# Kernel tuning notes

Hardware: AMD Instinct MI355X
Metric: run time of the kernel (lower is better)

The kernel has to match this reference:

```python
import jax, jax.numpy as jnp
import numpy as np
import math

HIDDEN = 768
KEY = 128      # attention_key_size
INTER = 1536   # intermediate_size
B, S = 4, 2048


def setup_inputs() -> dict:
    key = jax.random.key(0)
    ks = jax.random.split(key, 8)
    hidden_states = jax.random.normal(ks[0], (B, S, HIDDEN), dtype=jnp.float32)
    attention_mask = jax.random.randint(ks[1], (B, 1, 1, S), 0, 2, dtype=jnp.int32)
    position_ids = jnp.arange(B * S, dtype=jnp.int32).reshape(B, S) % S
    Wi = jax.random.normal(ks[2], (HIDDEN, 2 * INTER + KEY), dtype=jnp.float32) * 0.02
    bi = jnp.zeros((2 * INTER + KEY,), dtype=jnp.float32)
    gamma = jax.random.normal(ks[3], (2, KEY), dtype=jnp.float32) * 0.02 + 1.0
    beta = jnp.zeros((2, KEY), dtype=jnp.float32)
    Wo = jax.random.normal(ks[4], (INTER, HIDDEN), dtype=jnp.float32) * 0.02
    bo = jnp.zeros((HIDDEN,), dtype=jnp.float32)
    return {"hidden_states": hidden_states, "attention_mask": attention_mask,
            "position_ids": position_ids, "Wi": Wi, "bi": bi,
            "gamma": gamma, "beta": beta, "Wo": Wo, "bo": bo}


def _gau_forward(hidden_states, attention_mask, Wi, bi, gamma, beta, Wo, bo):
    # i_dense + swish activation
    h = jax.nn.silu(jnp.einsum('bsd,de->bse', hidden_states, Wi) + bi)
    u = h[..., :INTER]
    v = h[..., INTER:2 * INTER]
    qk = h[..., 2 * INTER:]
    # OffsetScale: per-head affine (heads=2 -> q, k)
    q = qk * gamma[0] + beta[0]
    k = qk * gamma[1] + beta[1]
    scores = jnp.einsum('bid,bjd->bij', q, k) / math.sqrt(KEY)
    # additive mask: (1 - m) * -1e12, squeeze head dim
    am = (1.0 - attention_mask.astype(scores.dtype)) * -1e12
    scores = scores + am[:, 0]  # [B,1,S] broadcasts over query dim
    # softmax_plus normalization: scale logits by log(l)/log(512)
    valid = (scores > -1e11).astype(scores.dtype)
    l = jnp.maximum(jnp.sum(valid, axis=-1, keepdims=True), 1.0)
    scale = jnp.log(l) / jnp.log(jnp.asarray(512.0, scores.dtype))
    attn = jax.nn.softmax(scores * scale, axis=-1)
    ctx = jnp.einsum('bij,bjd->bid', attn, v)
    return jnp.einsum('bse,eh->bsh', u * ctx, Wo) + bo


def reference(hidden_states, attention_mask, position_ids, Wi, bi, gamma, beta, Wo, bo):
    # position_ids unused: p_bias is not 'rotary'
    return _gau_forward(hidden_states, attention_mask, Wi, bi, gamma, beta, Wo, bo)
```

## Files before the change

### kernel.cpp

```cpp
#include <hip/hip_runtime.h>
#include <math.h>

#define HIDDEN 768
#define KEY    128
#define INTER  1536
#define NB     4
#define SEQ    2048
#define MTOT   (NB*SEQ)
#define ETOT   (2*INTER+KEY)
#define CS     136

typedef short bf16x8 __attribute__((ext_vector_type(8)));
typedef float f32x4  __attribute__((ext_vector_type(4)));
typedef unsigned short u16x8 __attribute__((ext_vector_type(8)));

__device__ __forceinline__ unsigned short f2bfbits(float x) {
    union { float f; unsigned int u; } a; a.f = x;
    unsigned int r = a.u + 0x7fffu + ((a.u >> 16) & 1u);
    return (unsigned short)(r >> 16);
}
__device__ __forceinline__ float bfbits2f(unsigned short b) {
    union { float f; unsigned int u; } a; a.u = ((unsigned int)b) << 16;
    return a.f;
}

__device__ __forceinline__ void gl2lds16(const unsigned short* g, unsigned short* l) {
    __builtin_amdgcn_global_load_lds(
        (const __attribute__((address_space(1))) unsigned int*)g,
        (__attribute__((address_space(3))) unsigned int*)l, 16, 0, 0);
}

__device__ __forceinline__ void transpose_tile(
    const float* __restrict__ in, unsigned short* __restrict__ out,
    int R, int C, int c0, int r0, int tid, unsigned short tile[32][33])
{
    int tx = tid & 31, ty4 = (tid >> 5)*4;
    #pragma unroll
    for (int rr = 0; rr < 4; rr++) {
        int r = ty4 + rr;
        tile[r][tx] = f2bfbits(in[(size_t)(r0+r)*C + c0+tx]);
    }
    __syncthreads();
    #pragma unroll
    for (int rr = 0; rr < 4; rr++) {
        int r = ty4 + rr;
        out[(size_t)(c0+r)*R + r0+tx] = tile[tx][r];
    }
}

__global__ __launch_bounds__(256) void prep_kernel(
    const float* __restrict__ X, const float* __restrict__ Wi,
    const float* __restrict__ Wo, const int* __restrict__ mask,
    unsigned short* __restrict__ Xb, unsigned short* __restrict__ WiT,
    unsigned short* __restrict__ WoT, float* __restrict__ scaleb)
{
    __shared__ unsigned short tile[32][33];
    __shared__ int red[256];
    const int bid = blockIdx.x, tid = threadIdx.x;
    if (bid < 3072) {
        int i = bid*256 + tid;
        const float4* in4 = (const float4*)X;
        float4 a = in4[(size_t)i*2], b = in4[(size_t)i*2+1];
        u16x8 o;
        o[0]=f2bfbits(a.x); o[1]=f2bfbits(a.y); o[2]=f2bfbits(a.z); o[3]=f2bfbits(a.w);
        o[4]=f2bfbits(b.x); o[5]=f2bfbits(b.y); o[6]=f2bfbits(b.z); o[7]=f2bfbits(b.w);
        *(u16x8*)&Xb[(size_t)i*8] = o;
    } else if (bid < 5472) {
        int t = bid - 3072;
        transpose_tile(Wi, WiT, HIDDEN, ETOT, (t%100)*32, (t/100)*32, tid, tile);
    } else if (bid < 6624) {
        int t = bid - 5472;
        transpose_tile(Wo, WoT, INTER, HIDDEN, (t%24)*32, (t/24)*32, tid, tile);
    } else {
        int b = bid - 6624;
        int s = 0;
        for (int j = tid; j < SEQ; j += 256)
            s += (mask[b*SEQ + j] != 0) ? 1 : 0;
        red[tid] = s;
        __syncthreads();
        for (int step = 128; step > 0; step >>= 1) {
            if (tid < step) red[tid] += red[tid + step];
            __syncthreads();
        }
        if (tid == 0) {
            float l = fmaxf((float)red[0], 1.0f);
            scaleb[b] = logf(l) / logf(512.0f);
        }
    }
}

template<int BK>
__device__ __forceinline__ void mfma_core(
    const unsigned short* __restrict__ Abase, int lda,
    const unsigned short* __restrict__ Bbase, int ldb,
    unsigned short* As, unsigned short* Bs,
    f32x4 acc[4][4], int tid, int ktot)
{
    const int lane = tid & 63, wave = tid >> 6;
    const int wm = (wave >> 1) << 6, wn = (wave & 1) << 6;
    const int lm = lane & 15;
    const int q8 = (lane >> 4) << 3;
    const int row_a = tid >> 2, col_a = (tid & 3) << 3;
    const int row_b = row_a + 64;

    for (int k0 = 0; k0 < ktot; k0 += BK) {
        if (k0) __syncthreads();
        #pragma unroll
        for (int h = 0; h < BK/32; h++) {
            gl2lds16(Abase + (size_t)row_a*lda + k0 + h*32 + col_a, As + h*4096 + tid*8);
            gl2lds16(Abase + (size_t)row_b*lda + k0 + h*32 + col_a, As + h*4096 + (tid+256)*8);
            gl2lds16(Bbase + (size_t)row_a*ldb + k0 + h*32 + col_a, Bs + h*4096 + tid*8);
            gl2lds16(Bbase + (size_t)row_b*ldb + k0 + h*32 + col_a, Bs + h*4096 + (tid+256)*8);
        }
        __syncthreads();
        #pragma unroll
        for (int h = 0; h < BK/32; h++) {
            const unsigned short* Ah = As + h*4096;
            const unsigned short* Bh = Bs + h*4096;
            bf16x8 af[4], bfr[4];
            #pragma unroll
            for (int i = 0; i < 4; i++)
                af[i] = *(const bf16x8*)&Ah[(wm + i*16 + lm)*32 + q8];
            #pragma unroll
            for (int j = 0; j < 4; j++)
                bfr[j] = *(const bf16x8*)&Bh[(wn + j*16 + lm)*32 + q8];
            #pragma unroll
            for (int i = 0; i < 4; i++)
                #pragma unroll
                for (int j = 0; j < 4; j++)
                    acc[i][j] = __builtin_amdgcn_mfma_f32_16x16x32_bf16(af[i], bfr[j], acc[i][j], 0, 0, 0);
        }
    }
}

#define EPILOG_IDX \
    const int lane = tid & 63, wave = tid >> 6; \
    const int wm = (wave >> 1) << 6, wn = (wave & 1) << 6; \
    const int cn = lane & 15, r4 = (lane >> 4) << 2;

__global__ __launch_bounds__(256) void gemm1_mfma(
    const unsigned short* __restrict__ Xb, const unsigned short* __restrict__ WiT,
    const float* __restrict__ bi, const float* __restrict__ gamma, const float* __restrict__ beta,
    unsigned short* __restrict__ u, unsigned short* __restrict__ vT,
    unsigned short* __restrict__ qb, unsigned short* __restrict__ kb)
{
    __shared__ __align__(16) unsigned short smem[128*CS];
    unsigned short* As = smem;
    unsigned short* Bs = smem + 4096;
    const int tid = threadIdx.x;
    const int bid = blockIdx.x;
    const int xcd = bid & 7, slot = bid >> 3;
    const int xt = slot >> 3;
    const int yt = (xcd << 3) + (slot & 7);
    const int row0 = yt*128, col0 = xt*128;
    f32x4 acc[4][4];
    #pragma unroll
    for (int i = 0; i < 4; i++)
        #pragma unroll
        for (int j = 0; j < 4; j++)
            acc[i][j] = (f32x4){0.f,0.f,0.f,0.f};
    mfma_core<32>(Xb + (size_t)row0*HIDDEN, HIDDEN, WiT + (size_t)col0*HIDDEN, HIDDEN,
                  As, Bs, acc, tid, HIDDEN);
    EPILOG_IDX
    __syncthreads();
    #pragma unroll
    for (int j = 0; j < 4; j++) {
        int nl = wn + j*16 + cn;
        float bin = bi[col0 + nl];
        #pragma unroll
        for (int i = 0; i < 4; i++) {
            #pragma unroll
            for (int r = 0; r < 4; r++) {
                int rowl = wm + i*16 + r4 + r;
                float x = acc[i][j][r] + bin;
                float h = x / (1.0f + __expf(-x));
                smem[rowl*CS + nl] = f2bfbits(h);
            }
        }
    }
    __syncthreads();
    if (col0 < INTER) {
        #pragma unroll
        for (int rnd = 0; rnd < 8; rnd++) {
            int row = rnd*16 + (tid>>4);
            int col = (tid&15)*8;
            u16x8 h = *(const u16x8*)&smem[row*CS + col];
            *(u16x8*)&u[(size_t)(row0+row)*INTER + col0 + col] = h;
        }
    } else if (col0 < 2*INTER) {
        int c = tid >> 1;
        int half = tid & 1;
        int b = row0 / SEQ;
        int srow = row0 - b*SEQ + half*64;
        size_t base = ((size_t)b*INTER + (col0 - INTER) + c)*SEQ + srow;
        #pragma unroll
        for (int k = 0; k < 8; k++) {
            u16x8 h;
            #pragma unroll
            for (int t = 0; t < 8; t++)
                h[t] = smem[(half*64 + k*8 + t)*CS + c];
            *(u16x8*)&vT[base + k*8] = h;
        }
    } else {
        #pragma unroll
        for (int rnd = 0; rnd < 8; rnd++) {
            int row = rnd*16 + (tid>>4);
            int col = (tid&15)*8;
            u16x8 h = *(const u16x8*)&smem[row*CS + col];
            int m = row0 + row;
            u16x8 qo, ko;
            #pragma unroll
            for (int t = 0; t < 8; t++) {
                float hv = bfbits2f(h[t]);
                qo[t] = f2bfbits(hv*gamma[col+t]     + beta[col+t]);
                ko[t] = f2bfbits(hv*gamma[KEY+col+t] + beta[KEY+col+t]);
            }
            *(u16x8*)&qb[(size_t)m*KEY + col] = qo;
            *(u16x8*)&kb[(size_t)m*KEY + col] = ko;
        }
    }
}

__global__ __launch_bounds__(256) void attn_mfma(
    const unsigned short* __restrict__ qb, const unsigned short* __restrict__ kb,
    const int* __restrict__ mask, const float* __restrict__ scaleb,
    unsigned short* __restrict__ P, float* __restrict__ lpart)
{
    __shared__ __align__(16) unsigned short smem[128*CS];
    unsigned short* As = smem;
    unsigned short* Bs = smem + 8192;
    const int tid = threadIdx.x;
    const int z = blockIdx.z;
    const int row0 = blockIdx.y*128, col0 = blockIdx.x*128;
    f32x4 acc[4][4];
    #pragma unroll
    for (int i = 0; i < 4; i++)
        #pragma unroll
        for (int j = 0; j < 4; j++)
            acc[i][j] = (f32x4){0.f,0.f,0.f,0.f};
    mfma_core<64>(qb + ((size_t)z*SEQ + row0)*KEY, KEY, kb + ((size_t)z*SEQ + col0)*KEY, KEY,
                  As, Bs, acc, tid, KEY);
    const float st = scaleb[z] * 0.08838834764831845f;
    EPILOG_IDX
    __syncthreads();
    #pragma unroll
    for (int j = 0; j < 4; j++) {
        int nl = wn + j*16 + cn;
        float mkf = (mask[z*SEQ + col0 + nl] != 0) ? 1.0f : 0.0f;
        #pragma unroll
        for (int i = 0; i < 4; i++) {
            #pragma unroll
            for (int r = 0; r < 4; r++) {
                int rowl = wm + i*16 + r4 + r;
                float p = mkf * __expf(acc[i][j][r]*st);
                smem[rowl*CS + nl] = f2bfbits(p);
            }
        }
    }
    __syncthreads();
    #pragma unroll
    for (int rnd = 0; rnd < 8; rnd++) {
        int row = rnd*16 + (tid>>4);
        int col = (tid&15)*8;
        u16x8 h = *(const u16x8*)&smem[row*CS + col];
        *(u16x8*)&P[((size_t)z*SEQ + row0 + row)*SEQ + col0 + col] = h;
        float s8 = 0.f;
        #pragma unroll
        for (int t = 0; t < 8; t++) s8 += bfbits2f(h[t]);
        #pragma unroll
        for (int off = 8; off > 0; off >>= 1) s8 += __shfl_xor(s8, off, 16);
        if ((tid & 15) == 0)
            lpart[(size_t)blockIdx.x*MTOT + (size_t)z*SEQ + row0 + row] = s8;
    }
}

__global__ __launch_bounds__(256) void pv_mfma(
    const unsigned short* __restrict__ P, const unsigned short* __restrict__ vT,
    const float* __restrict__ lpart, unsigned short* __restrict__ u)
{
    __shared__ __align__(16) unsigned short smem[128*CS];
    __shared__ float ls[128];
    unsigned short* As = smem;
    unsigned short* Bs = smem + 8192;
    const int tid = threadIdx.x;
    const int bid = blockIdx.x;
    const int xcd = bid & 7, slot = bid >> 3;
    const int z = slot / 24, pos = slot % 24;
    const int yt = (xcd & 3)*4 + pos/6;
    const int xt = (xcd >> 2)*6 + pos%6;
    const int row0 = yt*128, col0 = xt*128;
    if (tid < 128) {
        float s = 0.f;
        #pragma unroll
        for (int t = 0; t < 16; t++)
            s += lpart[(size_t)t*MTOT + (size_t)z*SEQ + row0 + tid];
        ls[tid] = s;
    }
    f32x4 acc[4][4];
    #pragma unroll
    for (int i = 0; i < 4; i++)
        #pragma unroll
        for (int j = 0; j < 4; j++)
            acc[i][j] = (f32x4){0.f,0.f,0.f,0.f};
    mfma_core<64>(P + ((size_t)z*SEQ + row0)*SEQ, SEQ, vT + ((size_t)z*INTER + col0)*SEQ, SEQ,
                  As, Bs, acc, tid, SEQ);
    EPILOG_IDX
    __syncthreads();
    #pragma unroll
    for (int j = 0; j < 4; j++) {
        int nl = wn + j*16 + cn;
        #pragma unroll
        for (int i = 0; i < 4; i++) {
            #pragma unroll
            for (int r = 0; r < 4; r++) {
                int rowl = wm + i*16 + r4 + r;
                smem[rowl*CS + nl] = f2bfbits(acc[i][j][r]);
            }
        }
    }
    __syncthreads();
    #pragma unroll
    for (int rnd = 0; rnd < 8; rnd++) {
        int row = rnd*16 + (tid>>4);
        int col = (tid&15)*8;
        int m = z*SEQ + row0 + row;
        float linv = 1.0f / ls[row];
        u16x8 cx = *(const u16x8*)&smem[row*CS + col];
        size_t idx = (size_t)m*INTER + col0 + col;
        u16x8 uu = *(const u16x8*)&u[idx];
        u16x8 g;
        #pragma unroll
        for (int t = 0; t < 8; t++)
            g[t] = f2bfbits(bfbits2f(uu[t]) * bfbits2f(cx[t]) * linv);
        *(u16x8*)&u[idx] = g;
    }
}

__global__ __launch_bounds__(256, 3) void gemm2_mfma(
    const unsigned short* __restrict__ g, const unsigned short* __restrict__ WoT,
    const float* __restrict__ bo, float* __restrict__ out)
{
    __shared__ __align__(16) unsigned short As[8192];
    __shared__ __align__(16) unsigned short Bs[4096];
    const int tid = threadIdx.x;
    const int bid = blockIdx.x;
    const int xcd = bid & 7, slot = bid >> 3;
    const int xt = slot >> 3;
    const int yt = (xcd << 3) + (slot & 7);
    const int row0 = yt*128, col0 = xt*64;
    const int lane = tid & 63, wave = tid >> 6;
    const int wm = (wave >> 1) << 6;
    const int wn = (wave & 1) << 5;
    const int lm = lane & 15;
    const int q8 = (lane >> 4) << 3;
    const int row_a = tid >> 2, col_a = (tid & 3) << 3;
    f32x4 acc[4][2];
    #pragma unroll
    for (int i = 0; i < 4; i++)
        #pragma unroll
        for (int j = 0; j < 2; j++)
            acc[i][j] = (f32x4){0.f,0.f,0.f,0.f};
    const unsigned short* Abase = g + (size_t)row0*INTER;
    const unsigned short* Bbase = WoT + (size_t)col0*INTER;
    for (int k0 = 0; k0 < INTER; k0 += 64) {
        if (k0) __syncthreads();
        #pragma unroll
        for (int h = 0; h < 2; h++) {
            gl2lds16(Abase + (size_t)row_a*INTER + k0 + h*32 + col_a,      As + h*4096 + tid*8);
            gl2lds16(Abase + (size_t)(row_a+64)*INTER + k0 + h*32 + col_a, As + h*4096 + (tid+256)*8);
            gl2lds16(Bbase + (size_t)row_a*INTER + k0 + h*32 + col_a,      Bs + h*2048 + tid*8);
        }
        __syncthreads();
        #pragma unroll
        for (int h = 0; h < 2; h++) {
            const unsigned short* Ah = As + h*4096;
            const unsigned short* Bh = Bs + h*2048;
            bf16x8 af[4], bfr[2];
            #pragma unroll
            for (int i = 0; i < 4; i++)
                af[i] = *(const bf16x8*)&Ah[(wm + i*16 + lm)*32 + q8];
            #pragma unroll
            for (int j = 0; j < 2; j++)
                bfr[j] = *(const bf16x8*)&Bh[(wn + j*16 + lm)*32 + q8];
            #pragma unroll
            for (int i = 0; i < 4; i++)
                #pragma unroll
                for (int j = 0; j < 2; j++)
                    acc[i][j] = __builtin_amdgcn_mfma_f32_16x16x32_bf16(af[i], bfr[j], acc[i][j], 0, 0, 0);
        }
    }
    const int cn = lane & 15, r4 = (lane >> 4) << 2;
    #pragma unroll
    for (int j = 0; j < 2; j++) {
        int n = col0 + wn + j*16 + cn;
        float bon = bo[n];
        #pragma unroll
        for (int i = 0; i < 4; i++) {
            #pragma unroll
            for (int r = 0; r < 4; r++) {
                int m = row0 + wm + i*16 + r4 + r;
                out[(size_t)m*HIDDEN + n] = acc[i][j][r] + bon;
            }
        }
    }
}

extern "C" void kernel_launch(void* const* d_in, const int* in_sizes, int n_in,
                              void* d_out, int out_size, void* d_ws, size_t ws_size,
                              hipStream_t stream)
{
    const float* X     = (const float*)d_in[0];
    const int*   mask  = (const int*)d_in[1];
    const float* Wi    = (const float*)d_in[3];
    const float* bi    = (const float*)d_in[4];
    const float* gamma = (const float*)d_in[5];
    const float* beta  = (const float*)d_in[6];
    const float* Wo    = (const float*)d_in[7];
    const float* bo    = (const float*)d_in[8];
    float* out = (float*)d_out;

    unsigned short* Xb  = (unsigned short*)d_ws;
    unsigned short* WiT = Xb  + (size_t)MTOT*HIDDEN;
    unsigned short* WoT = WiT + (size_t)ETOT*HIDDEN;
    unsigned short* u   = WoT + (size_t)HIDDEN*INTER;
    unsigned short* vT  = u   + (size_t)MTOT*INTER;
    unsigned short* qb  = vT  + (size_t)MTOT*INTER;
    unsigned short* kb  = qb  + (size_t)MTOT*KEY;
    unsigned short* P   = kb  + (size_t)MTOT*KEY;
    float* scb   = (float*)(P + (size_t)NB*SEQ*SEQ);
    float* lpart = scb + 8;

    prep_kernel<<<6628, 256, 0, stream>>>(X, Wi, Wo, mask, Xb, WiT, WoT, scb);
    gemm1_mfma<<<1600, 256, 0, stream>>>(Xb, WiT, bi, gamma, beta, u, vT, qb, kb);
    attn_mfma<<<dim3(SEQ/128, SEQ/128, NB), 256, 0, stream>>>(qb, kb, mask, scb, P, lpart);
    pv_mfma<<<768, 256, 0, stream>>>(P, vT, lpart, u);
    gemm2_mfma<<<768, 256, 0, stream>>>(u, WoT, bo, out);
}
```

Baseline: 289.3 us.

## Replace LDS-staged GEMM mainloops with direct global-to-register double-buffered loads

All four MFMA GEMM kernels drop shared-memory staging through global_load_lds and barriers. Each wave now loads its own A/B fragments straight from global memory into registers, with a two-step software prefetch across k. This removes LDS traffic and per-tile __syncthreads. In exchange, operands shared between waves are no longer reused through LDS, so global/L2 traffic rises, and each lane does strided 16-byte row loads instead of coalesced ones.

```diff
diff --git a/kernel.cpp b/kernel.cpp
--- a/kernel.cpp
+++ b/kernel.cpp
@@ -22,12 +22,6 @@
 __device__ __forceinline__ float bfbits2f(unsigned short b) {
     union { float f; unsigned int u; } a; a.u = ((unsigned int)b) << 16;
     return a.f;
-}
-
-__device__ __forceinline__ void gl2lds16(const unsigned short* g, unsigned short* l) {
-    __builtin_amdgcn_global_load_lds(
-        (const __attribute__((address_space(1))) unsigned int*)g,
-        (__attribute__((address_space(3))) unsigned int*)l, 16, 0, 0);
 }
 
 __device__ __forceinline__ void transpose_tile(
@@ -89,47 +83,50 @@
     }
 }
 
-template<int BK>
-__device__ __forceinline__ void mfma_core(
-    const unsigned short* __restrict__ Abase, int lda,
-    const unsigned short* __restrict__ Bbase, int ldb,
-    unsigned short* As, unsigned short* Bs,
-    f32x4 acc[4][4], int tid, int ktot)
+template<int NJ>
+__device__ __forceinline__ void mfma_direct(
+    const unsigned short* __restrict__ A, int lda,
+    const unsigned short* __restrict__ B, int ldb,
+    f32x4 acc[4][NJ], int tid, int ktot)
 {
     const int lane = tid & 63, wave = tid >> 6;
-    const int wm = (wave >> 1) << 6, wn = (wave & 1) << 6;
-    const int lm = lane & 15;
-    const int q8 = (lane >> 4) << 3;
-    const int row_a = tid >> 2, col_a = (tid & 3) << 3;
-    const int row_b = row_a + 64;
-
-    for (int k0 = 0; k0 < ktot; k0 += BK) {
-        if (k0) __syncthreads();
-        #pragma unroll
-        for (int h = 0; h < BK/32; h++) {
-            gl2lds16(Abase + (size_t)row_a*lda + k0 + h*32 + col_a, As + h*4096 + tid*8);
-            gl2lds16(Abase + (size_t)row_b*lda + k0 + h*32 + col_a, As + h*4096 + (tid+256)*8);
-            gl2lds16(Bbase + (size_t)row_a*ldb + k0 + h*32 + col_a, Bs + h*4096 + tid*8);
-            gl2lds16(Bbase + (size_t)row_b*ldb + k0 + h*32 + col_a, Bs + h*4096 + (tid+256)*8);
-        }
-        __syncthreads();
-        #pragma unroll
-        for (int h = 0; h < BK/32; h++) {
-            const unsigned short* Ah = As + h*4096;
-            const unsigned short* Bh = Bs + h*4096;
-            bf16x8 af[4], bfr[4];
-            #pragma unroll
-            for (int i = 0; i < 4; i++)
-                af[i] = *(const bf16x8*)&Ah[(wm + i*16 + lm)*32 + q8];
-            #pragma unroll
-            for (int j = 0; j < 4; j++)
-                bfr[j] = *(const bf16x8*)&Bh[(wn + j*16 + lm)*32 + q8];
-            #pragma unroll
-            for (int i = 0; i < 4; i++)
-                #pragma unroll
-                for (int j = 0; j < 4; j++)
-                    acc[i][j] = __builtin_amdgcn_mfma_f32_16x16x32_bf16(af[i], bfr[j], acc[i][j], 0, 0, 0);
-        }
+    const int wm = (wave >> 1) << 6;
+    const int wn = (wave & 1) * (NJ * 16);
+    const int lm = lane & 15, q8 = (lane >> 4) << 3;
+    const unsigned short* pa[4];
+    const unsigned short* pb[NJ];
+    #pragma unroll
+    for (int i = 0; i < 4; i++) pa[i] = A + (size_t)(wm + i*16 + lm)*lda + q8;
+    #pragma unroll
+    for (int j = 0; j < NJ; j++) pb[j] = B + (size_t)(wn + j*16 + lm)*ldb + q8;
+
+    bf16x8 ac[4], bc[NJ], an[4], bn[NJ];
+    #pragma unroll
+    for (int i = 0; i < 4; i++) ac[i] = *(const bf16x8*)(pa[i]);
+    #pragma unroll
+    for (int j = 0; j < NJ; j++) bc[j] = *(const bf16x8*)(pb[j]);
+
+    for (int k0 = 0; k0 < ktot; k0 += 64) {
+        #pragma unroll
+        for (int i = 0; i < 4; i++) an[i] = *(const bf16x8*)(pa[i] + k0 + 32);
+        #pragma unroll
+        for (int j = 0; j < NJ; j++) bn[j] = *(const bf16x8*)(pb[j] + k0 + 32);
+        #pragma unroll
+        for (int i = 0; i < 4; i++)
+            #pragma unroll
+            for (int j = 0; j < NJ; j++)
+                acc[i][j] = __builtin_amdgcn_mfma_f32_16x16x32_bf16(ac[i], bc[j], acc[i][j], 0, 0, 0);
+        if (k0 + 64 < ktot) {
+            #pragma unroll
+            for (int i = 0; i < 4; i++) ac[i] = *(const bf16x8*)(pa[i] + k0 + 64);
+            #pragma unroll
+            for (int j = 0; j < NJ; j++) bc[j] = *(const bf16x8*)(pb[j] + k0 + 64);
+        }
+        #pragma unroll
+        for (int i = 0; i < 4; i++)
+            #pragma unroll
+            for (int j = 0; j < NJ; j++)
+                acc[i][j] = __builtin_amdgcn_mfma_f32_16x16x32_bf16(an[i], bn[j], acc[i][j], 0, 0, 0);
     }
 }
 
@@ -145,8 +142,6 @@
     unsigned short* __restrict__ qb, unsigned short* __restrict__ kb)
 {
     __shared__ __align__(16) unsigned short smem[128*CS];
-    unsigned short* As = smem;
-    unsigned short* Bs = smem + 4096;
     const int tid = threadIdx.x;
     const int bid = blockIdx.x;
     const int xcd = bid & 7, slot = bid >> 3;
@@ -159,10 +154,9 @@
         #pragma unroll
         for (int j = 0; j < 4; j++)
             acc[i][j] = (f32x4){0.f,0.f,0.f,0.f};
-    mfma_core<32>(Xb + (size_t)row0*HIDDEN, HIDDEN, WiT + (size_t)col0*HIDDEN, HIDDEN,
-                  As, Bs, acc, tid, HIDDEN);
+    mfma_direct<4>(Xb + (size_t)row0*HIDDEN, HIDDEN, WiT + (size_t)col0*HIDDEN, HIDDEN,
+                   acc, tid, HIDDEN);
     EPILOG_IDX
-    __syncthreads();
     #pragma unroll
     for (int j = 0; j < 4; j++) {
         int nl = wn + j*16 + cn;
@@ -227,8 +221,6 @@
     unsigned short* __restrict__ P, float* __restrict__ lpart)
 {
     __shared__ __align__(16) unsigned short smem[128*CS];
-    unsigned short* As = smem;
-    unsigned short* Bs = smem + 8192;
     const int tid = threadIdx.x;
     const int z = blockIdx.z;
     const int row0 = blockIdx.y*128, col0 = blockIdx.x*128;
@@ -238,11 +230,10 @@
         #pragma unroll
         for (int j = 0; j < 4; j++)
             acc[i][j] = (f32x4){0.f,0.f,0.f,0.f};
-    mfma_core<64>(qb + ((size_t)z*SEQ + row0)*KEY, KEY, kb + ((size_t)z*SEQ + col0)*KEY, KEY,
-                  As, Bs, acc, tid, KEY);
+    mfma_direct<4>(qb + ((size_t)z*SEQ + row0)*KEY, KEY, kb + ((size_t)z*SEQ + col0)*KEY, KEY,
+                   acc, tid, KEY);
     const float st = scaleb[z] * 0.08838834764831845f;
     EPILOG_IDX
-    __syncthreads();
     #pragma unroll
     for (int j = 0; j < 4; j++) {
         int nl = wn + j*16 + cn;
@@ -280,8 +271,6 @@
 {
     __shared__ __align__(16) unsigned short smem[128*CS];
     __shared__ float ls[128];
-    unsigned short* As = smem;
-    unsigned short* Bs = smem + 8192;
     const int tid = threadIdx.x;
     const int bid = blockIdx.x;
     const int xcd = bid & 7, slot = bid >> 3;
@@ -302,10 +291,9 @@
         #pragma unroll
         for (int j = 0; j < 4; j++)
             acc[i][j] = (f32x4){0.f,0.f,0.f,0.f};
-    mfma_core<64>(P + ((size_t)z*SEQ + row0)*SEQ, SEQ, vT + ((size_t)z*INTER + col0)*SEQ, SEQ,
-                  As, Bs, acc, tid, SEQ);
+    mfma_direct<4>(P + ((size_t)z*SEQ + row0)*SEQ, SEQ, vT + ((size_t)z*INTER + col0)*SEQ, SEQ,
+                   acc, tid, SEQ);
     EPILOG_IDX
-    __syncthreads();
     #pragma unroll
     for (int j = 0; j < 4; j++) {
         int nl = wn + j*16 + cn;
@@ -336,59 +324,27 @@
     }
 }
 
-__global__ __launch_bounds__(256, 3) void gemm2_mfma(
+__global__ __launch_bounds__(256) void gemm2_mfma(
     const unsigned short* __restrict__ g, const unsigned short* __restrict__ WoT,
     const float* __restrict__ bo, float* __restrict__ out)
 {
-    __shared__ __align__(16) unsigned short As[8192];
-    __shared__ __align__(16) unsigned short Bs[4096];
     const int tid = threadIdx.x;
     const int bid = blockIdx.x;
     const int xcd = bid & 7, slot = bid >> 3;
     const int xt = slot >> 3;
     const int yt = (xcd << 3) + (slot & 7);
     const int row0 = yt*128, col0 = xt*64;
+    f32x4 acc[4][2];
+    #pragma unroll
+    for (int i = 0; i < 4; i++)
+        #pragma unroll
+        for (int j = 0; j < 2; j++)
+            acc[i][j] = (f32x4){0.f,0.f,0.f,0.f};
+    mfma_direct<2>(g + (size_t)row0*INTER, INTER, WoT + (size_t)col0*INTER, INTER,
+                   acc, tid, INTER);
     const int lane = tid & 63, wave = tid >> 6;
     const int wm = (wave >> 1) << 6;
     const int wn = (wave & 1) << 5;
-    const int lm = lane & 15;
-    const int q8 = (lane >> 4) << 3;
-    const int row_a = tid >> 2, col_a = (tid & 3) << 3;
-    f32x4 acc[4][2];
-    #pragma unroll
-    for (int i = 0; i < 4; i++)
-        #pragma unroll
-        for (int j = 0; j < 2; j++)
-            acc[i][j] = (f32x4){0.f,0.f,0.f,0.f};
-    const unsigned short* Abase = g + (size_t)row0*INTER;
-    const unsigned short* Bbase = WoT + (size_t)col0*INTER;
-    for (int k0 = 0; k0 < INTER; k0 += 64) {
-        if (k0) __syncthreads();
-        #pragma unroll
-        for (int h = 0; h < 2; h++) {
-            gl2lds16(Abase + (size_t)row_a*INTER + k0 + h*32 + col_a,      As + h*4096 + tid*8);
-            gl2lds16(Abase + (size_t)(row_a+64)*INTER + k0 + h*32 + col_a, As + h*4096 + (tid+256)*8);
-            gl2lds16(Bbase + (size_t)row_a*INTER + k0 + h*32 + col_a,      Bs + h*2048 + tid*8);
-        }
-        __syncthreads();
-        #pragma unroll
-        for (int h = 0; h < 2; h++) {
-            const unsigned short* Ah = As + h*4096;
-            const unsigned short* Bh = Bs + h*2048;
-            bf16x8 af[4], bfr[2];
-            #pragma unroll
-            for (int i = 0; i < 4; i++)
-                af[i] = *(const bf16x8*)&Ah[(wm + i*16 + lm)*32 + q8];
-            #pragma unroll
-            for (int j = 0; j < 2; j++)
-                bfr[j] = *(const bf16x8*)&Bh[(wn + j*16 + lm)*32 + q8];
-            #pragma unroll
-            for (int i = 0; i < 4; i++)
-                #pragma unroll
-                for (int j = 0; j < 2; j++)
-                    acc[i][j] = __builtin_amdgcn_mfma_f32_16x16x32_bf16(af[i], bfr[j], acc[i][j], 0, 0, 0);
-        }
-    }
     const int cn = lane & 15, r4 = (lane >> 4) << 2;
     #pragma unroll
     for (int j = 0; j < 2; j++) {
```

Result: slower. 558.1 us (+92.9%).
